# Optimization experiments

Measured on AMD Instinct MI355X. Metric: run time of the kernel, lower is better.

Reference implementation:

```python
import jax, jax.numpy as jnp
import numpy as np

IMG = 640
NUM_CLASSES = 80
STRIDES = (8, 16, 32)
CONF_THRESH = 0.05
NMS_THRESH = 0.5
C3, C4, C5 = 128, 256, 512
B = 4


def _conv(x, w, b, pad):
    # x: [B,Cin,H,W], w: [Cout,Cin,kh,kw]
    y = jax.lax.conv_general_dilated(x, w, (1, 1), [(pad, pad), (pad, pad)],
                                     dimension_numbers=('NCHW', 'OIHW', 'NCHW'))
    return y + b[None, :, None, None]


def _conv_act(x, w, b):
    return jax.nn.leaky_relu(_conv(x, w, b, 1), 0.1)


def _head(x, ws, bs):
    # ws: [4,256,256,3,3] stacked head convs (fixed count of 4)
    for i in range(ws.shape[0]):
        x = _conv_act(x, ws[i], bs[i])
    return x


def _up2(x):
    # nearest-neighbor upsample x2 (F.interpolate default)
    return jnp.repeat(jnp.repeat(x, 2, axis=2), 2, axis=3)


def _grid(stride):
    hs = IMG // stride
    gy, gx = jnp.meshgrid(jnp.arange(hs), jnp.arange(hs), indexing='ij')
    return jnp.stack([gx, gy], -1).reshape(-1, 2).astype(jnp.float32)  # [hs*ws,2]


def _fcos_dense(c3, c4, c5, params):
    (lat1_w, lat1_b, lat2_w, lat2_b, lat3_w, lat3_b,
     sm1_w, sm1_b, sm2_w, sm2_b, sm3_w, sm3_b,
     clsh_w, clsh_b, regh_w, regh_b,
     cls_det_w, cls_det_b, reg_det_w, reg_det_b, ctn_det_w, ctn_det_b) = params
    p5 = _conv(c5, lat3_w, lat3_b, 0)
    p5_up = _up2(p5)                      # upsample BEFORE smooth, as in source
    p5 = _conv(p5, sm3_w, sm3_b, 1)
    p4 = _conv(c4, lat2_w, lat2_b, 0) + p5_up
    p4_up = _up2(p4)
    p4 = _conv(p4, sm2_w, sm2_b, 1)
    p3 = _conv(_conv(c3, lat1_w, lat1_b, 0) + p4_up, sm1_w, sm1_b, 1)
    cls_all, box_all, ctn_all = [], [], []
    for p, s in zip((p3, p4, p5), STRIDES):
        bsz = p.shape[0]
        ch = _head(p, clsh_w, clsh_b)
        rh = _head(p, regh_w, regh_b)
        cls_i = jnp.transpose(_conv(ch, cls_det_w, cls_det_b, 0), (0, 2, 3, 1)).reshape(bsz, -1, NUM_CLASSES)
        reg_i = jnp.transpose(_conv(rh, reg_det_w, reg_det_b, 0), (0, 2, 3, 1)).reshape(bsz, -1, 4)
        ctn_i = jnp.transpose(_conv(rh, ctn_det_w, ctn_det_b, 0), (0, 2, 3, 1)).reshape(bsz, -1, 1)
        g = _grid(s)[None]                 # [1,HW,2]
        x1y1 = (g - jnp.exp(reg_i[..., :2])) * s
        x2y2 = (g + jnp.exp(reg_i[..., 2:])) * s
        cls_all.append(cls_i)
        box_all.append(jnp.concatenate([x1y1, x2y2], -1))
        ctn_all.append(ctn_i)
    return (jnp.concatenate(cls_all, 1), jnp.concatenate(box_all, 1), jnp.concatenate(ctn_all, 1))


def _nms_keep(boxes, scores, cls_inds):
    # Greedy per-class NMS, fixed-shape: returns keep mask in original order.
    N = boxes.shape[0]
    order = jnp.argsort(-scores)
    b = boxes[order]
    s = scores[order]
    c = cls_inds[order]
    x1, y1, x2, y2 = b[:, 0], b[:, 1], b[:, 2], b[:, 3]
    areas = (x2 - x1) * (y2 - y1)
    idx = jnp.arange(N)
    keep0 = s >= CONF_THRESH

    def body(i, keep):
        xx1 = jnp.maximum(x1[i], x1)
        yy1 = jnp.maximum(y1[i], y1)
        xx2 = jnp.minimum(x2[i], x2)
        yy2 = jnp.minimum(y2[i], y2)
        w = jnp.maximum(1e-28, xx2 - xx1)
        h = jnp.maximum(1e-28, yy2 - yy1)
        inter = w * h
        ovr = inter / (areas[i] + areas - inter)
        sup = keep[i] & (idx > i) & (c == c[i]) & (ovr > NMS_THRESH)
        return keep & ~sup

    keep = jax.lax.fori_loop(0, N, body, keep0)
    return jnp.zeros(N, bool).at[order].set(keep)


def setup_inputs() -> dict:
    key = jax.random.key(0)
    ks = iter(jax.random.split(key, 64))

    def wn(shape):
        fan_in = float(np.prod(shape[1:]))
        return jax.random.normal(next(ks), shape, jnp.float32) / np.sqrt(fan_in)

    def bz(n):
        return jnp.zeros((n,), jnp.float32)

    inp = {
        'c3': jax.random.normal(next(ks), (B, C3, 80, 80), jnp.float32),
        'c4': jax.random.normal(next(ks), (B, C4, 40, 40), jnp.float32),
        'c5': jax.random.normal(next(ks), (B, C5, 20, 20), jnp.float32),
        'lat1_w': wn((256, C3, 1, 1)), 'lat1_b': bz(256),
        'lat2_w': wn((256, C4, 1, 1)), 'lat2_b': bz(256),
        'lat3_w': wn((256, C5, 1, 1)), 'lat3_b': bz(256),
        'sm1_w': wn((256, 256, 3, 3)), 'sm1_b': bz(256),
        'sm2_w': wn((256, 256, 3, 3)), 'sm2_b': bz(256),
        'sm3_w': wn((256, 256, 3, 3)), 'sm3_b': bz(256),
        'clsh_w': jnp.stack([wn((256, 256, 3, 3)) for _ in range(4)]),
        'clsh_b': jnp.zeros((4, 256), jnp.float32),
        'regh_w': jnp.stack([wn((256, 256, 3, 3)) for _ in range(4)]),
        'regh_b': jnp.zeros((4, 256), jnp.float32),
        'cls_det_w': wn((NUM_CLASSES, 256, 1, 1)),
        'cls_det_b': jnp.full((NUM_CLASSES,), -np.log(99.0), jnp.float32),
        'reg_det_w': wn((4, 256, 1, 1)), 'reg_det_b': bz(4),
        'ctn_det_w': wn((1, 256, 1, 1)), 'ctn_det_b': bz(1),
    }
    return inp


def reference(c3, c4, c5, lat1_w, lat1_b, lat2_w, lat2_b, lat3_w, lat3_b,
              sm1_w, sm1_b, sm2_w, sm2_b, sm3_w, sm3_b,
              clsh_w, clsh_b, regh_w, regh_b,
              cls_det_w, cls_det_b, reg_det_w, reg_det_b, ctn_det_w, ctn_det_b):
    params = (lat1_w, lat1_b, lat2_w, lat2_b, lat3_w, lat3_b,
              sm1_w, sm1_b, sm2_w, sm2_b, sm3_w, sm3_b,
              clsh_w, clsh_b, regh_w, regh_b,
              cls_det_w, cls_det_b, reg_det_w, reg_det_b, ctn_det_w, ctn_det_b)
    cls_pred, box_pred, ctn_pred = _fcos_dense(c3, c4, c5, params)
    scores = jnp.sqrt(jax.nn.sigmoid(cls_pred) * jax.nn.sigmoid(ctn_pred))[0]  # [N,C]
    bboxes = jnp.clip(box_pred / IMG, 0.0, 1.0)[0]                              # [N,4]
    cls_inds = jnp.argmax(scores, axis=1)
    best = jnp.take_along_axis(scores, cls_inds[:, None], axis=1)[:, 0]
    keep = _nms_keep(bboxes, best, cls_inds)
    return bboxes, best, cls_inds.astype(jnp.int32), keep
```

## Files before the change

kernel.cpp:

```cpp
#include <hip/hip_runtime.h>
#include <stdint.h>

#define CONF_T 0.05f
#define NMS_T  0.5f
#define WMAX   132
#define WSTEP9 589824

typedef _Float16 f16x8 __attribute__((ext_vector_type(8)));
typedef _Float16 f16x2 __attribute__((ext_vector_type(2)));
typedef float    f32x4 __attribute__((ext_vector_type(4)));
#define MFMA16 __builtin_amdgcn_mfma_f32_16x16x32_f16

#define OFF_T3   0u
#define OFF_T4   1638400u
#define OFF_T5   2048000u
#define OFF_P3   2150400u
#define OFF_P4   3788800u
#define OFF_P5   4198400u
#define OFF_HA3  4300800u
#define OFF_HA4  5939200u
#define OFF_HA5  6348800u
#define OFF_HB3  6451200u
#define OFF_HB4  8089600u
#define OFF_HB5  8499200u
#define OFF_HD3  8601600u
#define OFF_HD4  10240000u
#define OFF_HD5  10649600u
#define OFF_CLS  10752000u
#define OFF_REG  11424000u
#define OFF_CTN  11457600u
#define OFF_W2H  11466000u
#define OFF_W2L  14710032u
#define WS_NEED  17954064u
#define POFF_KEYS  (OFF_T3 + 0u)
#define POFF_SCS   (OFF_T3 + 32768u)
#define POFF_CLSS  (OFF_T3 + 49152u)
#define POFF_IDXS  (OFF_T3 + 65536u)
#define POFF_GX1   (OFF_T3 + 81920u)
#define POFF_GY1   (OFF_T3 + 90320u)
#define POFF_GX2   (OFF_T3 + 98720u)
#define POFF_GY2   (OFF_T3 + 107120u)
#define POFF_GAR   (OFF_T3 + 115520u)
#define POFF_GIX   (OFF_T3 + 123920u)
#define POFF_NCNT  (OFF_T3 + 132320u)
#define POFF_NBASE (OFF_T3 + 132400u)
#define POFF_CROW  (OFF_T3 + 132480u)
#define POFF_NZ    (OFF_T3 + 140880u)
#define POFF_MASK  OFF_HA3

__launch_bounds__(256)
__global__ void conv1x1_kernel(const float* __restrict__ in, const float* __restrict__ w,
                               const float* __restrict__ b, float* __restrict__ out,
                               const float* __restrict__ add,
                               int Cin, int Cout, int NPX, int W, int outStride, int outBase)
{
    __shared__ float s_in[16][64];
    __shared__ float s_w[16][64];
    int t = threadIdx.x;
    int pxg = t & 31, cg = t >> 5;
    int px0 = blockIdx.x * 64;
    int co0 = blockIdx.y * 64;
    float acc[8][2];
#pragma unroll
    for (int c = 0; c < 8; ++c) { acc[c][0] = 0.f; acc[c][1] = 0.f; }
    int chunks = Cin >> 4;
    int wco = t >> 2, wpart = t & 3;
    for (int ch = 0; ch < chunks; ++ch) {
        int ci0 = ch << 4;
#pragma unroll
        for (int k = 0; k < 4; ++k) {
            int id = t + k * 256;
            int ci = id >> 6, pp = id & 63;
            int gp = px0 + pp;
            s_in[ci][pp] = (gp < NPX) ? in[(size_t)(ci0 + ci) * NPX + gp] : 0.f;
        }
        {
            int gco = co0 + wco;
            if (gco < Cout) {
                const float* run = w + (size_t)gco * Cin + ci0;
#pragma unroll
                for (int k = 0; k < 4; ++k) {
                    int e = wpart + 4 * k;
                    s_w[e][wco] = run[e];
                }
            } else {
#pragma unroll
                for (int k = 0; k < 4; ++k) s_w[wpart + 4 * k][wco] = 0.f;
            }
        }
        __syncthreads();
#pragma unroll
        for (int ci = 0; ci < 16; ++ci) {
            float i0 = s_in[ci][pxg * 2], i1 = s_in[ci][pxg * 2 + 1];
#pragma unroll
            for (int c = 0; c < 8; ++c) {
                float wv = s_w[ci][cg * 8 + c];
                acc[c][0] += wv * i0;
                acc[c][1] += wv * i1;
            }
        }
        __syncthreads();
    }
    for (int c = 0; c < 8; ++c) {
        int co = co0 + cg * 8 + c;
        if (co >= Cout) break;
        float bb = b[co];
#pragma unroll
        for (int j = 0; j < 2; ++j) {
            int p = px0 + pxg * 2 + j;
            if (p < NPX) {
                float v = acc[c][j] + bb;
                if (add) {
                    int y = p / W, x = p % W;
                    int Sp = W >> 1;
                    v += add[(size_t)co * (Sp * Sp) + (y >> 1) * Sp + (x >> 1)];
                }
                out[(size_t)co * outStride + outBase + p] = v;
            }
        }
    }
}

struct Det9 {
    const float* src[9]; const float* w[9]; const float* b[9];
    float*       dst[9];
    int cout[9], npx[9], obase[9], bstart[9], npxb[9];
};

__launch_bounds__(256)
__global__ void det1x1_fused(Det9 d)
{
    int bid = blockIdx.x;
    int q = 0;
#pragma unroll
    for (int i = 1; i < 9; ++i) if (bid >= d.bstart[i]) q = i;
    int local = bid - d.bstart[q];
    int coIdx = local / d.npxb[q];
    int pxIdx = local - coIdx * d.npxb[q];
    const float* in = d.src[q];
    const float* w  = d.w[q];
    const float* b  = d.b[q];
    float* out = d.dst[q];
    int Cout = d.cout[q], NPX = d.npx[q], outBase = d.obase[q];

    __shared__ float s_in[16][64];
    __shared__ float s_w[16][64];
    int t = threadIdx.x;
    int pxg = t & 31, cg = t >> 5;
    int px0 = pxIdx * 64;
    int co0 = coIdx * 64;
    float acc[8][2];
#pragma unroll
    for (int c = 0; c < 8; ++c) { acc[c][0] = 0.f; acc[c][1] = 0.f; }
    int wco = t >> 2, wpart = t & 3;
    for (int ch = 0; ch < 16; ++ch) {
        int ci0 = ch << 4;
#pragma unroll
        for (int k = 0; k < 4; ++k) {
            int id = t + k * 256;
            int ci = id >> 6, pp = id & 63;
            int gp = px0 + pp;
            s_in[ci][pp] = (gp < NPX) ? in[(size_t)(ci0 + ci) * NPX + gp] : 0.f;
        }
        {
            int gco = co0 + wco;
            if (gco < Cout) {
                const float* run = w + (size_t)gco * 256 + ci0;
#pragma unroll
                for (int k = 0; k < 4; ++k) {
                    int e = wpart + 4 * k;
                    s_w[e][wco] = run[e];
                }
            } else {
#pragma unroll
                for (int k = 0; k < 4; ++k) s_w[wpart + 4 * k][wco] = 0.f;
            }
        }
        __syncthreads();
#pragma unroll
        for (int ci = 0; ci < 16; ++ci) {
            float i0 = s_in[ci][pxg * 2], i1 = s_in[ci][pxg * 2 + 1];
#pragma unroll
            for (int c = 0; c < 8; ++c) {
                float wv = s_w[ci][cg * 8 + c];
                acc[c][0] += wv * i0;
                acc[c][1] += wv * i1;
            }
        }
        __syncthreads();
    }
    for (int c = 0; c < 8; ++c) {
        int co = co0 + cg * 8 + c;
        if (co >= Cout) break;
        float bb = b[co];
#pragma unroll
        for (int j = 0; j < 2; ++j) {
            int p = px0 + pxg * 2 + j;
            if (p < NPX) out[(size_t)co * 8400 + outBase + p] = acc[c][j] + bb;
        }
    }
}

__launch_bounds__(256)
__global__ void w2prep(const float* __restrict__ clsh_w, const float* __restrict__ regh_w,
                       const float* __restrict__ sm1_w, const float* __restrict__ sm2_w,
                       const float* __restrict__ sm3_w,
                       _Float16* __restrict__ WH, _Float16* __restrict__ WL)
{
    int idx = blockIdx.x * 256 + threadIdx.x;
    if (idx >= 11 * WSTEP9) return;
    int m = idx / WSTEP9, e = idx - m * WSTEP9;
    int tap = e / 65536;
    int r   = e - tap * 65536;
    int cob = r / 4096;
    int r2  = r - cob * 4096;
    int ck  = r2 / 512;
    int r3  = r2 - ck * 512;
    int lane = r3 / 8, el = r3 - (r3 / 8) * 8;
    int co = cob * 16 + (lane & 15);
    int ci = ck * 32 + (lane >> 4) * 8 + el;
    const float* srcb;
    if (m < 4)       srcb = clsh_w + (size_t)m * WSTEP9;
    else if (m < 8)  srcb = regh_w + (size_t)(m - 4) * WSTEP9;
    else if (m == 8) srcb = sm1_w;
    else if (m == 9) srcb = sm2_w;
    else             srcb = sm3_w;
    float f = srcb[(size_t)co * 2304 + ci * 9 + tap];
    _Float16 h = (_Float16)f;
    _Float16 l = (_Float16)(f - (float)h);
    WH[idx] = h; WL[idx] = l;
}

struct MC {
    const float*    src[2][3];
    float*          dst[2][3];
    const _Float16* wh[2][3];
    const _Float16* wl[2][3];
    const float*    bias[2][3];
    int act;
    int nbr;
};

__launch_bounds__(256)
__global__ void mconv3x3(MC p)
{
    __shared__ __align__(16) _Float16 SH[2][108 * 40];
    __shared__ __align__(16) _Float16 SL[2][108 * 40];
    int t = threadIdx.x;
    int NS = 4 * p.nbr;
    int bid = blockIdx.x;
    int slice = bid % NS;
    int sp = bid / NS;
    int br = slice % p.nbr;
    int co0 = (slice / p.nbr) * 64;
    int lvl = (sp < 100) ? 0 : (sp < 130) ? 1 : 2;
    int tloc = sp - ((lvl == 0) ? 0 : (lvl == 1) ? 100 : 130);
    int W = (lvl == 0) ? 80 : (lvl == 1) ? 40 : 20;
    int nTx = (lvl == 0) ? 5 : (lvl == 1) ? 3 : 2;
    int HW = W * W;
    int bx0 = (tloc % nTx) * 16, by0 = (tloc / nTx) * 4;
    const float* src = p.src[br][lvl];
    float* dst = p.dst[br][lvl];
    const _Float16* wh = p.wh[br][lvl];
    const _Float16* wl = p.wl[br][lvl];
    const float* bias = p.bias[br][lvl];

    int lane = t & 63, wid = t >> 6;
    int cw = wid & 1, pw = wid >> 1;
    int colc = lane & 15, g = lane >> 4;

    int sgo[7], sla[7];
#pragma unroll
    for (int k = 0; k < 7; ++k) {
        int s2 = t + k * 256;
        sgo[k] = -1; sla[k] = 0;
        if (s2 < 1728) {
            int ci2 = s2 / 108, cell = s2 - ci2 * 108;
            int r = cell / 18, c = cell - r * 18;
            sla[k] = cell * 40 + ci2 * 2;
            int gy = by0 - 1 + r, gx = bx0 - 1 + c;
            if (gy >= 0 && gy < W && gx >= 0 && gx < W)
                sgo[k] = (ci2 * 2) * HW + gy * W + gx;
        }
    }

    f32x4 acc[2][2];
#pragma unroll
    for (int mi = 0; mi < 2; ++mi)
#pragma unroll
        for (int ny = 0; ny < 2; ++ny) acc[mi][ny] = (f32x4)0.f;

#pragma unroll
    for (int k = 0; k < 7; ++k) {
        if (t + k * 256 < 1728) {
            float v0 = 0.f, v1 = 0.f;
            if (sgo[k] >= 0) { v0 = src[sgo[k]]; v1 = src[sgo[k] + HW]; }
            _Float16 h0 = (_Float16)v0, h1 = (_Float16)v1;
            _Float16 l0 = (_Float16)(v0 - (float)h0), l1 = (_Float16)(v1 - (float)h1);
            f16x2 ph = {h0, h1}, pl = {l0, l1};
            *(f16x2*)&SH[0][sla[k]] = ph;
            *(f16x2*)&SL[0][sla[k]] = pl;
        }
    }
    __syncthreads();

    int cob0 = (co0 + cw * 32) >> 4;
    auto aoff = [&](int ckk, int tap, int mi) -> size_t {
        return ((size_t)((tap * 16 + cob0 + mi) * 8 + ckk)) * 512 + lane * 8;
    };
    f16x8 Ah0[3], Al0[3], Ah1[3], Al1[3];
    {
        size_t a0 = aoff(0, 0, 0), a1 = aoff(0, 0, 1);
        Ah0[0] = *(const f16x8*)(wh + a0); Al0[0] = *(const f16x8*)(wl + a0);
        Ah1[0] = *(const f16x8*)(wh + a1); Al1[0] = *(const f16x8*)(wl + a1);
        a0 = aoff(0, 1, 0); a1 = aoff(0, 1, 1);
        Ah0[1] = *(const f16x8*)(wh + a0); Al0[1] = *(const f16x8*)(wl + a0);
        Ah1[1] = *(const f16x8*)(wh + a1); Al1[1] = *(const f16x8*)(wl + a1);
    }
    for (int ck = 0; ck < 8; ++ck) {
        const _Float16* sh  = SH[ck & 1];
        const _Float16* sl_ = SL[ck & 1];
        float pv[14];
        bool pf = (ck < 7);
        if (pf) {
            const float* sb = src + (size_t)(ck + 1) * 32 * HW;
#pragma unroll
            for (int k = 0; k < 7; ++k) {
                pv[2 * k] = 0.f; pv[2 * k + 1] = 0.f;
                if (t + k * 256 < 1728 && sgo[k] >= 0) {
                    pv[2 * k] = sb[sgo[k]]; pv[2 * k + 1] = sb[sgo[k] + HW];
                }
            }
        }
#pragma unroll
        for (int tap = 0; tap < 9; ++tap) {
            int ky = tap / 3, kx = tap - ky * 3;
            int slot = tap % 3;
            int nsl  = (tap + 2) % 3;
            int pck = ck, ptap = tap + 2;
            if (ptap >= 9) { ptap -= 9; if (pf) pck = ck + 1; }
            size_t an0 = aoff(pck, ptap, 0), an1 = aoff(pck, ptap, 1);
            Ah0[nsl] = *(const f16x8*)(wh + an0);
            Al0[nsl] = *(const f16x8*)(wl + an0);
            Ah1[nsl] = *(const f16x8*)(wh + an1);
            Al1[nsl] = *(const f16x8*)(wl + an1);
#pragma unroll
            for (int ny = 0; ny < 2; ++ny) {
                int cell = (pw * 2 + ny + ky) * 18 + colc + kx;
                f16x8 bh = *(const f16x8*)(sh  + cell * 40 + g * 8);
                f16x8 bl = *(const f16x8*)(sl_ + cell * 40 + g * 8);
                acc[0][ny] = MFMA16(Ah0[slot], bh, acc[0][ny], 0, 0, 0);
                acc[1][ny] = MFMA16(Ah1[slot], bh, acc[1][ny], 0, 0, 0);
                acc[0][ny] = MFMA16(Ah0[slot], bl, acc[0][ny], 0, 0, 0);
                acc[1][ny] = MFMA16(Ah1[slot], bl, acc[1][ny], 0, 0, 0);
                acc[0][ny] = MFMA16(Al0[slot], bh, acc[0][ny], 0, 0, 0);
                acc[1][ny] = MFMA16(Al1[slot], bh, acc[1][ny], 0, 0, 0);
            }
        }
        if (pf) {
            _Float16* nh = SH[(ck + 1) & 1];
            _Float16* nl = SL[(ck + 1) & 1];
#pragma unroll
            for (int k = 0; k < 7; ++k) {
                if (t + k * 256 < 1728) {
                    float v0 = pv[2 * k], v1 = pv[2 * k + 1];
                    _Float16 h0 = (_Float16)v0, h1 = (_Float16)v1;
                    _Float16 l0 = (_Float16)(v0 - (float)h0), l1 = (_Float16)(v1 - (float)h1);
                    f16x2 ph = {h0, h1}, pl = {l0, l1};
                    *(f16x2*)&nh[sla[k]] = ph;
                    *(f16x2*)&nl[sla[k]] = pl;
                }
            }
        }
        __syncthreads();
    }

    int x = bx0 + colc;
    if (x < W) {
#pragma unroll
        for (int mi = 0; mi < 2; ++mi) {
            int cob = co0 + cw * 32 + mi * 16 + g * 4;
#pragma unroll
            for (int ny = 0; ny < 2; ++ny) {
                int y = by0 + pw * 2 + ny;
#pragma unroll
                for (int i = 0; i < 4; ++i) {
                    int co = cob + i;
                    float v = acc[mi][ny][i] + bias[co];
                    if (p.act) v = (v >= 0.f) ? v : 0.1f * v;
                    dst[(size_t)co * HW + y * W + x] = v;
                }
            }
        }
    }
}

__launch_bounds__(256)
__global__ void decode_kernel(const float* __restrict__ cls, const float* __restrict__ reg,
                              const float* __restrict__ ctn, float* __restrict__ out,
                              unsigned long long* __restrict__ keys)
{
    int p = blockIdx.x * 256 + threadIdx.x;
    if (p >= 16384) return;
    if (p >= 8400) { keys[p] = ~0ull; return; }
    int base, hs; float s;
    if (p < 6400)      { base = 0;    hs = 80; s = 8.f;  }
    else if (p < 8000) { base = 6400; hs = 40; s = 16.f; }
    else               { base = 8000; hs = 20; s = 32.f; }
    int local = p - base;
    float gx = (float)(local % hs), gy = (float)(local / hs);
    float ct = ctn[p];
    float sct = 1.f / (1.f + expf(-ct));
    float best = -1.f; int arg = 0;
    for (int c = 0; c < 80; ++c) {
        float v = cls[(size_t)c * 8400 + p];
        float sv = 1.f / (1.f + expf(-v));
        float sc = sqrtf(sv * sct);
        if (sc > best) { best = sc; arg = c; }
    }
    float r0 = reg[0 * 8400 + p], r1 = reg[1 * 8400 + p];
    float r2 = reg[2 * 8400 + p], r3 = reg[3 * 8400 + p];
    float x1 = (gx - expf(r0)) * s / 640.f;
    float y1 = (gy - expf(r1)) * s / 640.f;
    float x2 = (gx + expf(r2)) * s / 640.f;
    float y2 = (gy + expf(r3)) * s / 640.f;
    x1 = fminf(fmaxf(x1, 0.f), 1.f);
    y1 = fminf(fmaxf(y1, 0.f), 1.f);
    x2 = fminf(fmaxf(x2, 0.f), 1.f);
    y2 = fminf(fmaxf(y2, 0.f), 1.f);
    out[p * 4 + 0] = x1; out[p * 4 + 1] = y1;
    out[p * 4 + 2] = x2; out[p * 4 + 3] = y2;
    out[33600 + p] = best;
    out[42000 + p] = (float)arg;
    out[50400 + p] = 0.f;
    unsigned int ub = __float_as_uint(best);
    keys[p] = ((unsigned long long)(~ub) << 32) | (unsigned int)p;
}

__launch_bounds__(256)
__global__ void bitonic_local(unsigned long long* __restrict__ keys, unsigned kmerge)
{
    __shared__ unsigned long long sk[2048];
    int t = threadIdx.x;
    unsigned base = blockIdx.x * 2048u;
#pragma unroll
    for (int m = 0; m < 8; ++m) sk[t + m * 256] = keys[base + t + m * 256];
    __syncthreads();
    if (kmerge == 0u) {
        for (unsigned k = 2; k <= 2048u; k <<= 1) {
            for (unsigned j = k >> 1; j > 0; j >>= 1) {
#pragma unroll
                for (int pp = 0; pp < 4; ++pp) {
                    unsigned p = (unsigned)t + pp * 256u;
                    unsigned li = ((p & ~(j - 1)) << 1) | (p & (j - 1));
                    unsigned gi = base + li;
                    bool up = ((gi & k) == 0);
                    unsigned long long a = sk[li], b = sk[li + j];
                    if ((a > b) == up) { sk[li] = b; sk[li + j] = a; }
                }
                __syncthreads();
            }
        }
    } else {
        unsigned k = kmerge;
        for (unsigned j = 1024; j > 0; j >>= 1) {
#pragma unroll
            for (int pp = 0; pp < 4; ++pp) {
                unsigned p = (unsigned)t + pp * 256u;
                unsigned li = ((p & ~(j - 1)) << 1) | (p & (j - 1));
                unsigned gi = base + li;
                bool up = ((gi & k) == 0);
                unsigned long long a = sk[li], b = sk[li + j];
                if ((a > b) == up) { sk[li] = b; sk[li + j] = a; }
            }
            __syncthreads();
        }
    }
#pragma unroll
    for (int m = 0; m < 8; ++m) keys[base + t + m * 256] = sk[t + m * 256];
}

__launch_bounds__(256)
__global__ void bitonic_global(unsigned long long* __restrict__ keys, unsigned k, unsigned j)
{
    unsigned p = blockIdx.x * 256u + threadIdx.x;
    unsigned i = ((p & ~(j - 1)) << 1) | (p & (j - 1));
    bool up = ((i & k) == 0);
    unsigned long long a = keys[i], b = keys[i + j];
    if ((a > b) == up) { keys[i] = b; keys[i + j] = a; }
}

__launch_bounds__(256)
__global__ void sorted_aux(const unsigned long long* __restrict__ keys,
                           const float* __restrict__ out,
                           float* __restrict__ scs, int* __restrict__ clss,
                           int* __restrict__ idxs)
{
    int i = blockIdx.x * 256 + threadIdx.x;
    if (i >= 16384) return;
    unsigned long long key = keys[i];
    unsigned ub = ~(unsigned)(key >> 32);
    float sc = __uint_as_float(ub);
    unsigned idx = (unsigned)(key & 0xffffffffu);
    int cl = -1;
    if (idx < 8400u) cl = (int)out[42000 + idx];
    else sc = 0.f;
    scs[i] = sc; clss[i] = cl; idxs[i] = (int)idx;
}

__launch_bounds__(256)
__global__ void compact_cls(const float* __restrict__ scs, const int* __restrict__ clss,
                            const int* __restrict__ idxs, const float* __restrict__ outbuf,
                            float* __restrict__ GX1, float* __restrict__ GY1,
                            float* __restrict__ GX2, float* __restrict__ GY2,
                            float* __restrict__ GAR, int* __restrict__ GIX,
                            int* __restrict__ CROW,
                            int* __restrict__ NCOUNT, int* __restrict__ NBASE)
{
    int c = blockIdx.x, t = threadIdx.x;
    __shared__ int s_red[2];
    __shared__ int s_wtot[4];
    int cb = 0, co = 0;
    for (int i = t; i < 16384; i += 256) {
        float sc = scs[i]; int cl = clss[i];
        if (sc >= CONF_T && cl >= 0) { cb += (cl < c); co += (cl == c); }
    }
    if (t == 0) { s_red[0] = 0; s_red[1] = 0; }
    __syncthreads();
    atomicAdd(&s_red[0], cb);
    atomicAdd(&s_red[1], co);
    __syncthreads();
    int base = s_red[0], n = s_red[1];
    if (t == 0) { NCOUNT[c] = n; NBASE[c] = base; }

    int rank = 0;
    for (int st = 0; st < 16384; st += 256) {
        int i = st + t;
        float sc = scs[i]; int cl = clss[i];
        bool flag = (sc >= CONF_T && cl == c);
        unsigned long long m = __ballot(flag);
        int lane = t & 63, wv = t >> 6;
        if (lane == 0) s_wtot[wv] = __popcll(m);
        __syncthreads();
        int off = rank;
        for (int w = 0; w < wv; ++w) off += s_wtot[w];
        int tot = s_wtot[0] + s_wtot[1] + s_wtot[2] + s_wtot[3];
        if (flag) {
            int pos = off + __popcll(m & ((1ull << lane) - 1ull));
            int idx = idxs[i];
            float x1 = outbuf[idx * 4 + 0], y1 = outbuf[idx * 4 + 1];
            float x2 = outbuf[idx * 4 + 2], y2 = outbuf[idx * 4 + 3];
            GX1[base + pos] = x1; GY1[base + pos] = y1;
            GX2[base + pos] = x2; GY2[base + pos] = y2;
            GAR[base + pos] = (x2 - x1) * (y2 - y1);
            GIX[base + pos] = idx;
            CROW[base + pos] = c;
        }
        rank += tot;
        __syncthreads();
    }
}

__launch_bounds__(256)
__global__ void nms_mask(const float* __restrict__ GX1, const float* __restrict__ GY1,
                         const float* __restrict__ GX2, const float* __restrict__ GY2,
                         const float* __restrict__ GAR,
                         const int* __restrict__ CROW,
                         const int* __restrict__ NCOUNT, const int* __restrict__ NBASE,
                         unsigned long long* __restrict__ MASK,
                         unsigned long long* __restrict__ NZ)
{
    int lane = threadIdx.x & 63, wid = threadIdx.x >> 6;
    int gr = blockIdx.x * 4 + wid;
    int tot = NBASE[79] + NCOUNT[79];
    if (gr >= tot) return;
    int c = CROW[gr];
    int base = NBASE[c], n = NCOUNT[c];
    int r = gr - base;
    float rx1 = GX1[gr], ry1 = GY1[gr];
    float rx2 = GX2[gr], ry2 = GY2[gr];
    float rar = GAR[gr];
    int Wc = (n + 63) >> 6;
    unsigned long long nz0 = 0ull, nz1 = 0ull, nz2 = 0ull;
    for (int w = 0; w < Wc; ++w) {
        int jb = w * 64;
        unsigned long long m = 0ull;
        if (jb + 63 > r) {
            int j = jb + lane;
            bool pred = false;
            if (j > r && j < n) {
                float xx1 = fmaxf(rx1, GX1[base + j]);
                float yy1 = fmaxf(ry1, GY1[base + j]);
                float xx2 = fminf(rx2, GX2[base + j]);
                float yy2 = fminf(ry2, GY2[base + j]);
                float ww = fmaxf(1e-28f, xx2 - xx1);
                float hh = fmaxf(1e-28f, yy2 - yy1);
                float inter = ww * hh;
                float ovr = inter / (rar + GAR[base + j] - inter);
                pred = (ovr > NMS_T);
            }
            m = __ballot(pred);
        }
        if (lane == 0) {
            MASK[(size_t)gr * WMAX + w] = m;
            if (m) {
                if (w < 64)       nz0 |= 1ull << w;
                else if (w < 128) nz1 |= 1ull << (w - 64);
                else              nz2 |= 1ull << (w - 128);
            }
        }
    }
    if (lane == 0) {
        NZ[(size_t)gr * 4 + 0] = nz0;
        NZ[(size_t)gr * 4 + 1] = nz1;
        NZ[(size_t)gr * 4 + 2] = nz2;
    }
}

__launch_bounds__(256)
__global__ void nms_scan(const unsigned long long* __restrict__ MASK,
                         const unsigned long long* __restrict__ NZ,
                         const int* __restrict__ GIX,
                         const int* __restrict__ NCOUNT, const int* __restrict__ NBASE,
                         float* __restrict__ keep)
{
    int c = blockIdx.x, t = threadIdx.x;
    int n = NCOUNT[c];
    if (n == 0) return;
    int base = NBASE[c];
    int Wc = (n + 63) >> 6;
    __shared__ unsigned long long remv[WMAX];
    __shared__ unsigned long long sdiag[64];
    __shared__ unsigned long long s_am;
    __shared__ int s_rows[64];
    __shared__ int s_na;
    for (int w = t; w < Wc; w += 256) remv[w] = 0ull;
    __syncthreads();
    for (int i0 = 0; i0 < n; i0 += 64) {
        int rows = min(64, n - i0);
        int wq = i0 >> 6;
        if (t < rows) sdiag[t] = MASK[(size_t)(base + i0 + t) * WMAX + wq];
        __syncthreads();
        if (t == 0) {
            unsigned long long live = (rows < 64) ? ((1ull << rows) - 1ull) : ~0ull;
            live &= ~remv[wq];
            unsigned long long am = 0ull;
            int na = 0;
            while (live) {
                int rr = __ffsll((unsigned long long)live) - 1;
                am |= 1ull << rr;
                s_rows[na++] = rr;
                live &= ~sdiag[rr];
                live &= ~(1ull << rr);
            }
            s_am = am; s_na = na;
        }
        __syncthreads();
        unsigned long long am = s_am;
        int na = s_na;
        if (t < na) {
            int gr = base + i0 + s_rows[t];
#pragma unroll
            for (int part = 0; part < 3; ++part) {
                unsigned long long nz = NZ[(size_t)gr * 4 + part];
                while (nz) {
                    int b = __ffsll((unsigned long long)nz) - 1;
                    nz &= nz - 1ull;
                    int w = part * 64 + b;
                    atomicOr(&remv[w], MASK[(size_t)gr * WMAX + w]);
                }
            }
        }
        __syncthreads();
        if (t < rows && ((am >> t) & 1ull)) keep[GIX[base + i0 + t]] = 1.0f;
        __syncthreads();
    }
}

extern "C" void kernel_launch(void* const* d_in, const int* in_sizes, int n_in,
                              void* d_out, int out_size, void* d_ws, size_t ws_size,
                              hipStream_t stream)
{
    const float* c3      = (const float*)d_in[0];
    const float* c4      = (const float*)d_in[1];
    const float* c5      = (const float*)d_in[2];
    const float* lat1_w  = (const float*)d_in[3];
    const float* lat1_b  = (const float*)d_in[4];
    const float* lat2_w  = (const float*)d_in[5];
    const float* lat2_b  = (const float*)d_in[6];
    const float* lat3_w  = (const float*)d_in[7];
    const float* lat3_b  = (const float*)d_in[8];
    const float* sm1_w   = (const float*)d_in[9];
    const float* sm1_b   = (const float*)d_in[10];
    const float* sm2_w   = (const float*)d_in[11];
    const float* sm2_b   = (const float*)d_in[12];
    const float* sm3_w   = (const float*)d_in[13];
    const float* sm3_b   = (const float*)d_in[14];
    const float* clsh_w  = (const float*)d_in[15];
    const float* clsh_b  = (const float*)d_in[16];
    const float* regh_w  = (const float*)d_in[17];
    const float* regh_b  = (const float*)d_in[18];
    const float* clsd_w  = (const float*)d_in[19];
    const float* clsd_b  = (const float*)d_in[20];
    const float* regd_w  = (const float*)d_in[21];
    const float* regd_b  = (const float*)d_in[22];
    const float* ctnd_w  = (const float*)d_in[23];
    const float* ctnd_b  = (const float*)d_in[24];

    float* ws = (float*)d_ws;
    float* T3 = ws + OFF_T3;  float* T4 = ws + OFF_T4;  float* T5 = ws + OFF_T5;
    float* P3 = ws + OFF_P3;  float* P4 = ws + OFF_P4;  float* P5 = ws + OFF_P5;
    float* HA3 = ws + OFF_HA3; float* HA4 = ws + OFF_HA4; float* HA5 = ws + OFF_HA5;
    float* HB3 = ws + OFF_HB3; float* HB4 = ws + OFF_HB4; float* HB5 = ws + OFF_HB5;
    float* HD3 = ws + OFF_HD3; float* HD4 = ws + OFF_HD4; float* HD5 = ws + OFF_HD5;
    float* CLS = ws + OFF_CLS; float* REG = ws + OFF_REG; float* CTN = ws + OFF_CTN;
    _Float16* WH = (_Float16*)(ws + OFF_W2H);
    _Float16* WL = (_Float16*)(ws + OFF_W2L);
    unsigned long long* KEYS = (unsigned long long*)(ws + POFF_KEYS);
    float* SCS = ws + POFF_SCS;
    int* CLSS = (int*)(ws + POFF_CLSS);
    int* IDXS = (int*)(ws + POFF_IDXS);
    float* GX1 = ws + POFF_GX1; float* GY1 = ws + POFF_GY1;
    float* GX2 = ws + POFF_GX2; float* GY2 = ws + POFF_GY2;
    float* GAR = ws + POFF_GAR;
    int* GIX = (int*)(ws + POFF_GIX);
    int* CROW = (int*)(ws + POFF_CROW);
    int* NCOUNT = (int*)(ws + POFF_NCNT);
    int* NBASE  = (int*)(ws + POFF_NBASE);
    unsigned long long* NZ = (unsigned long long*)(ws + POFF_NZ);
    unsigned long long* MASK = (unsigned long long*)(ws + POFF_MASK);

    float* out = (float*)d_out;
    dim3 blk(256);

    w2prep<<<dim3((11 * WSTEP9 + 255) / 256), blk, 0, stream>>>(
        clsh_w, regh_w, sm1_w, sm2_w, sm3_w, WH, WL);

    conv1x1_kernel<<<dim3(7, 4), blk, 0, stream>>>(c5, lat3_w, lat3_b, T5, nullptr,
                                                   512, 256, 400, 20, 400, 0);
    conv1x1_kernel<<<dim3(25, 4), blk, 0, stream>>>(c4, lat2_w, lat2_b, T4, T5,
                                                    256, 256, 1600, 40, 1600, 0);
    conv1x1_kernel<<<dim3(100, 4), blk, 0, stream>>>(c3, lat1_w, lat1_b, T3, T4,
                                                     128, 256, 6400, 80, 6400, 0);
    {
        MC mc{};
        float* sT[3] = {T3, T4, T5};
        float* sP[3] = {P3, P4, P5};
        const float* sB[3] = {sm1_b, sm2_b, sm3_b};
        for (int l = 0; l < 3; ++l) {
            mc.src[0][l] = sT[l]; mc.dst[0][l] = sP[l];
            mc.wh[0][l] = WH + (size_t)(8 + l) * WSTEP9;
            mc.wl[0][l] = WL + (size_t)(8 + l) * WSTEP9;
            mc.bias[0][l] = sB[l];
        }
        mc.act = 0; mc.nbr = 1;
        mconv3x3<<<dim3(140 * 4), blk, 0, stream>>>(mc);
    }
    {
        float* clsS[3][5] = { {P3, HA3, HB3, HA3, HB3},
                              {P4, HA4, HB4, HA4, HB4},
                              {P5, HA5, HB5, HA5, HB5} };
        float* regS[3][5] = { {P3, T3,  HD3, T3,  HD3},
                              {P4, T4,  HD4, T4,  HD4},
                              {P5, T5,  HD5, T5,  HD5} };
        for (int i = 0; i < 4; ++i) {
            MC mc{};
            for (int l = 0; l < 3; ++l) {
                mc.src[0][l] = clsS[l][i]; mc.dst[0][l] = clsS[l][i + 1];
                mc.src[1][l] = regS[l][i]; mc.dst[1][l] = regS[l][i + 1];
                mc.wh[0][l] = WH + (size_t)i * WSTEP9;
                mc.wl[0][l] = WL + (size_t)i * WSTEP9;
                mc.wh[1][l] = WH + (size_t)(4 + i) * WSTEP9;
                mc.wl[1][l] = WL + (size_t)(4 + i) * WSTEP9;
                mc.bias[0][l] = clsh_b + i * 256;
                mc.bias[1][l] = regh_b + i * 256;
            }
            mc.act = 1; mc.nbr = 2;
            mconv3x3<<<dim3(140 * 8), blk, 0, stream>>>(mc);
        }
    }

    {
        Det9 d;
        const float* feats[3][2] = { {HB3, HD3}, {HB4, HD4}, {HB5, HD5} };
        int   npx[3]   = {6400, 1600, 400};
        int   obase[3] = {0, 6400, 8000};
        int q = 0, bacc = 0;
        for (int l = 0; l < 3; ++l) {
            d.src[q] = feats[l][0]; d.w[q] = clsd_w; d.b[q] = clsd_b; d.dst[q] = CLS;
            d.cout[q] = 80; d.npx[q] = npx[l]; d.obase[q] = obase[l];
            d.bstart[q] = bacc; d.npxb[q] = (npx[l] + 63) / 64;
            bacc += d.npxb[q] * 2; ++q;
            d.src[q] = feats[l][1]; d.w[q] = regd_w; d.b[q] = regd_b; d.dst[q] = REG;
            d.cout[q] = 4; d.npx[q] = npx[l]; d.obase[q] = obase[l];
            d.bstart[q] = bacc; d.npxb[q] = (npx[l] + 63) / 64;
            bacc += d.npxb[q]; ++q;
            d.src[q] = feats[l][1]; d.w[q] = ctnd_w; d.b[q] = ctnd_b; d.dst[q] = CTN;
            d.cout[q] = 1; d.npx[q] = npx[l]; d.obase[q] = obase[l];
            d.bstart[q] = bacc; d.npxb[q] = (npx[l] + 63) / 64;
            bacc += d.npxb[q]; ++q;
        }
        det1x1_fused<<<dim3(bacc), blk, 0, stream>>>(d);
    }

    decode_kernel<<<dim3(64), blk, 0, stream>>>(CLS, REG, CTN, out, KEYS);

    bitonic_local<<<dim3(8), blk, 0, stream>>>(KEYS, 0u);
    bitonic_global<<<dim3(32), blk, 0, stream>>>(KEYS, 4096u, 2048u);
    bitonic_local<<<dim3(8), blk, 0, stream>>>(KEYS, 4096u);
    bitonic_global<<<dim3(32), blk, 0, stream>>>(KEYS, 8192u, 4096u);
    bitonic_global<<<dim3(32), blk, 0, stream>>>(KEYS, 8192u, 2048u);
    bitonic_local<<<dim3(8), blk, 0, stream>>>(KEYS, 8192u);
    bitonic_global<<<dim3(32), blk, 0, stream>>>(KEYS, 16384u, 8192u);
    bitonic_global<<<dim3(32), blk, 0, stream>>>(KEYS, 16384u, 4096u);
    bitonic_global<<<dim3(32), blk, 0, stream>>>(KEYS, 16384u, 2048u);
    bitonic_local<<<dim3(8), blk, 0, stream>>>(KEYS, 16384u);

    sorted_aux<<<dim3(64), blk, 0, stream>>>(KEYS, out, SCS, CLSS, IDXS);
    compact_cls<<<dim3(80), blk, 0, stream>>>(SCS, CLSS, IDXS, out,
                                              GX1, GY1, GX2, GY2, GAR, GIX, CROW,
                                              NCOUNT, NBASE);
    nms_mask<<<dim3(2100), blk, 0, stream>>>(GX1, GY1, GX2, GY2, GAR, CROW,
                                             NCOUNT, NBASE, MASK, NZ);
    nms_scan<<<dim3(80), blk, 0, stream>>>(MASK, NZ, GIX, NCOUNT, NBASE, out + 50400);
}
```

Measured before the change: 935.6 us.

## Store intermediate conv activations as pre-split fp16 hi/lo channel pairs

The 3x3 conv kernel can now write its output as packed fp16 high and low halves for channel pairs instead of fp32 planes. The next conv then loads these words straight into shared memory without converting again. This removes the repeated fp32-to-split-fp16 conversion during staging and keeps global traffic the same size (two 32-bit words per channel pair). The smooth convs and the first three head layers emit the pair layout, and the last head layer still writes fp32 for the detector kernel. The change relies on every buffer being large enough for the hi and lo planes placed at the 128*HW offset.

```diff
diff --git a/kernel.cpp b/kernel.cpp
--- a/kernel.cpp
+++ b/kernel.cpp
@@ -239,6 +239,8 @@
     const float*    bias[2][3];
     int act;
     int nbr;
+    int inPairs;
+    int outPairs;
 };
 
 __launch_bounds__(256)
@@ -264,23 +266,28 @@
     const _Float16* wh = p.wh[br][lvl];
     const _Float16* wl = p.wl[br][lvl];
     const float* bias = p.bias[br][lvl];
+    const unsigned* PHsrc = (const unsigned*)src;
+    const unsigned* PLsrc = PHsrc + (size_t)128 * HW;
 
     int lane = t & 63, wid = t >> 6;
     int cw = wid & 1, pw = wid >> 1;
     int colc = lane & 15, g = lane >> 4;
 
-    int sgo[7], sla[7];
+    int sgo[7], sci[7], sla[7];
 #pragma unroll
     for (int k = 0; k < 7; ++k) {
         int s2 = t + k * 256;
-        sgo[k] = -1; sla[k] = 0;
+        sgo[k] = -1; sci[k] = 0; sla[k] = 0;
         if (s2 < 1728) {
             int ci2 = s2 / 108, cell = s2 - ci2 * 108;
             int r = cell / 18, c = cell - r * 18;
             sla[k] = cell * 40 + ci2 * 2;
+            sci[k] = ci2;
             int gy = by0 - 1 + r, gx = bx0 - 1 + c;
             if (gy >= 0 && gy < W && gx >= 0 && gx < W)
-                sgo[k] = (ci2 * 2) * HW + gy * W + gx;
+                sgo[k] = gy * W + gx;
+        } else {
+            sla[k] = -1;
         }
     }
 
@@ -292,14 +299,23 @@
 
 #pragma unroll
     for (int k = 0; k < 7; ++k) {
-        if (t + k * 256 < 1728) {
-            float v0 = 0.f, v1 = 0.f;
-            if (sgo[k] >= 0) { v0 = src[sgo[k]]; v1 = src[sgo[k] + HW]; }
-            _Float16 h0 = (_Float16)v0, h1 = (_Float16)v1;
-            _Float16 l0 = (_Float16)(v0 - (float)h0), l1 = (_Float16)(v1 - (float)h1);
-            f16x2 ph = {h0, h1}, pl = {l0, l1};
-            *(f16x2*)&SH[0][sla[k]] = ph;
-            *(f16x2*)&SL[0][sla[k]] = pl;
+        if (sla[k] >= 0) {
+            unsigned hw_ = 0u, lw_ = 0u;
+            if (sgo[k] >= 0) {
+                if (p.inPairs) {
+                    hw_ = PHsrc[(size_t)sci[k] * HW + sgo[k]];
+                    lw_ = PLsrc[(size_t)sci[k] * HW + sgo[k]];
+                } else {
+                    float v0 = src[(size_t)(sci[k] * 2) * HW + sgo[k]];
+                    float v1 = src[(size_t)(sci[k] * 2 + 1) * HW + sgo[k]];
+                    _Float16 h0 = (_Float16)v0, h1 = (_Float16)v1;
+                    _Float16 l0 = (_Float16)(v0 - (float)h0), l1 = (_Float16)(v1 - (float)h1);
+                    f16x2 ph = {h0, h1}, pl = {l0, l1};
+                    hw_ = *(unsigned*)&ph; lw_ = *(unsigned*)&pl;
+                }
+            }
+            *(unsigned*)&SH[0][sla[k]] = hw_;
+            *(unsigned*)&SL[0][sla[k]] = lw_;
         }
     }
     __syncthreads();
@@ -320,21 +336,34 @@
     for (int ck = 0; ck < 8; ++ck) {
         const _Float16* sh  = SH[ck & 1];
         const _Float16* sl_ = SL[ck & 1];
-        float pv[14];
+        unsigned pv[14];
         bool pf = (ck < 7);
         if (pf) {
-            const float* sb = src + (size_t)(ck + 1) * 32 * HW;
-#pragma unroll
-            for (int k = 0; k < 7; ++k) {
-                pv[2 * k] = 0.f; pv[2 * k + 1] = 0.f;
-                if (t + k * 256 < 1728 && sgo[k] >= 0) {
-                    pv[2 * k] = sb[sgo[k]]; pv[2 * k + 1] = sb[sgo[k] + HW];
+            if (p.inPairs) {
+                const unsigned* ph = PHsrc + (size_t)(ck + 1) * 16 * HW;
+                const unsigned* pl = PLsrc + (size_t)(ck + 1) * 16 * HW;
+#pragma unroll
+                for (int k = 0; k < 7; ++k) {
+                    pv[2 * k] = 0u; pv[2 * k + 1] = 0u;
+                    if (sla[k] >= 0 && sgo[k] >= 0) {
+                        pv[2 * k]     = ph[(size_t)sci[k] * HW + sgo[k]];
+                        pv[2 * k + 1] = pl[(size_t)sci[k] * HW + sgo[k]];
+                    }
+                }
+            } else {
+                const float* sb = src + (size_t)(ck + 1) * 32 * HW;
+#pragma unroll
+                for (int k = 0; k < 7; ++k) {
+                    pv[2 * k] = 0u; pv[2 * k + 1] = 0u;
+                    if (sla[k] >= 0 && sgo[k] >= 0) {
+                        pv[2 * k]     = __float_as_uint(sb[(size_t)(sci[k] * 2) * HW + sgo[k]]);
+                        pv[2 * k + 1] = __float_as_uint(sb[(size_t)(sci[k] * 2 + 1) * HW + sgo[k]]);
+                    }
                 }
             }
         }
 #pragma unroll
         for (int tap = 0; tap < 9; ++tap) {
-            int ky = tap / 3, kx = tap - ky * 3;
             int slot = tap % 3;
             int nsl  = (tap + 2) % 3;
             int pck = ck, ptap = tap + 2;
@@ -344,6 +373,7 @@
             Al0[nsl] = *(const f16x8*)(wl + an0);
             Ah1[nsl] = *(const f16x8*)(wh + an1);
             Al1[nsl] = *(const f16x8*)(wl + an1);
+            int ky = tap / 3, kx = tap - ky * 3;
 #pragma unroll
             for (int ny = 0; ny < 2; ++ny) {
                 int cell = (pw * 2 + ny + ky) * 18 + colc + kx;
@@ -360,15 +390,26 @@
         if (pf) {
             _Float16* nh = SH[(ck + 1) & 1];
             _Float16* nl = SL[(ck + 1) & 1];
-#pragma unroll
-            for (int k = 0; k < 7; ++k) {
-                if (t + k * 256 < 1728) {
-                    float v0 = pv[2 * k], v1 = pv[2 * k + 1];
-                    _Float16 h0 = (_Float16)v0, h1 = (_Float16)v1;
-                    _Float16 l0 = (_Float16)(v0 - (float)h0), l1 = (_Float16)(v1 - (float)h1);
-                    f16x2 ph = {h0, h1}, pl = {l0, l1};
-                    *(f16x2*)&nh[sla[k]] = ph;
-                    *(f16x2*)&nl[sla[k]] = pl;
+            if (p.inPairs) {
+#pragma unroll
+                for (int k = 0; k < 7; ++k) {
+                    if (sla[k] >= 0) {
+                        *(unsigned*)&nh[sla[k]] = pv[2 * k];
+                        *(unsigned*)&nl[sla[k]] = pv[2 * k + 1];
+                    }
+                }
+            } else {
+#pragma unroll
+                for (int k = 0; k < 7; ++k) {
+                    if (sla[k] >= 0) {
+                        float v0 = __uint_as_float(pv[2 * k]);
+                        float v1 = __uint_as_float(pv[2 * k + 1]);
+                        _Float16 h0 = (_Float16)v0, h1 = (_Float16)v1;
+                        _Float16 l0 = (_Float16)(v0 - (float)h0), l1 = (_Float16)(v1 - (float)h1);
+                        f16x2 ph = {h0, h1}, pl = {l0, l1};
+                        *(unsigned*)&nh[sla[k]] = *(unsigned*)&ph;
+                        *(unsigned*)&nl[sla[k]] = *(unsigned*)&pl;
+                    }
                 }
             }
         }
@@ -377,18 +418,37 @@
 
     int x = bx0 + colc;
     if (x < W) {
+        unsigned* PHdst = (unsigned*)dst;
+        unsigned* PLdst = PHdst + (size_t)128 * HW;
 #pragma unroll
         for (int mi = 0; mi < 2; ++mi) {
             int cob = co0 + cw * 32 + mi * 16 + g * 4;
 #pragma unroll
             for (int ny = 0; ny < 2; ++ny) {
                 int y = by0 + pw * 2 + ny;
+                int off = y * W + x;
+                float v[4];
 #pragma unroll
                 for (int i = 0; i < 4; ++i) {
-                    int co = cob + i;
-                    float v = acc[mi][ny][i] + bias[co];
-                    if (p.act) v = (v >= 0.f) ? v : 0.1f * v;
-                    dst[(size_t)co * HW + y * W + x] = v;
+                    float vv = acc[mi][ny][i] + bias[cob + i];
+                    if (p.act) vv = (vv >= 0.f) ? vv : 0.1f * vv;
+                    v[i] = vv;
+                }
+                if (p.outPairs) {
+#pragma unroll
+                    for (int pr = 0; pr < 2; ++pr) {
+                        float v0 = v[2 * pr], v1 = v[2 * pr + 1];
+                        _Float16 h0 = (_Float16)v0, h1 = (_Float16)v1;
+                        _Float16 l0 = (_Float16)(v0 - (float)h0), l1 = (_Float16)(v1 - (float)h1);
+                        f16x2 ph = {h0, h1}, pl = {l0, l1};
+                        size_t pidx = (size_t)(cob / 2 + pr) * HW + off;
+                        PHdst[pidx] = *(unsigned*)&ph;
+                        PLdst[pidx] = *(unsigned*)&pl;
+                    }
+                } else {
+#pragma unroll
+                    for (int i = 0; i < 4; ++i)
+                        dst[(size_t)(cob + i) * HW + off] = v[i];
                 }
             }
         }
@@ -753,7 +813,7 @@
             mc.wl[0][l] = WL + (size_t)(8 + l) * WSTEP9;
             mc.bias[0][l] = sB[l];
         }
-        mc.act = 0; mc.nbr = 1;
+        mc.act = 0; mc.nbr = 1; mc.inPairs = 0; mc.outPairs = 1;
         mconv3x3<<<dim3(140 * 4), blk, 0, stream>>>(mc);
     }
     {
@@ -776,6 +836,8 @@
                 mc.bias[1][l] = regh_b + i * 256;
             }
             mc.act = 1; mc.nbr = 2;
+            mc.inPairs = 1;
+            mc.outPairs = (i < 3) ? 1 : 0;
             mconv3x3<<<dim3(140 * 8), blk, 0, stream>>>(mc);
         }
     }
```

Result: slower. 993.2 us (+6.2%).

## Halve 3x3 conv spatial tile to two rows, one 16-channel block per wave

Applied to the files above, without the earlier changes.

The 3x3 MFMA conv tile shrinks from 16x4 to 16x2 output pixels per block, and each wave now owns a distinct 16-output-channel block instead of a 32-channel by 2-row share. The block count doubles and LDS per block drops, which should raise occupancy and spread work over more CUs. In exchange, each wave fetches its own weights with less reuse across pixels, and halo overhead per output pixel goes up (4 input rows for 2 output rows).

```diff
diff --git a/kernel.cpp b/kernel.cpp
--- a/kernel.cpp
+++ b/kernel.cpp
@@ -244,8 +244,8 @@
 __launch_bounds__(256)
 __global__ void mconv3x3(MC p)
 {
-    __shared__ __align__(16) _Float16 SH[2][108 * 40];
-    __shared__ __align__(16) _Float16 SL[2][108 * 40];
+    __shared__ __align__(16) _Float16 SH[2][72 * 40];
+    __shared__ __align__(16) _Float16 SL[2][72 * 40];
     int t = threadIdx.x;
     int NS = 4 * p.nbr;
     int bid = blockIdx.x;
@@ -253,12 +253,12 @@
     int sp = bid / NS;
     int br = slice % p.nbr;
     int co0 = (slice / p.nbr) * 64;
-    int lvl = (sp < 100) ? 0 : (sp < 130) ? 1 : 2;
-    int tloc = sp - ((lvl == 0) ? 0 : (lvl == 1) ? 100 : 130);
+    int lvl = (sp < 200) ? 0 : (sp < 260) ? 1 : 2;
+    int tloc = sp - ((lvl == 0) ? 0 : (lvl == 1) ? 200 : 260);
     int W = (lvl == 0) ? 80 : (lvl == 1) ? 40 : 20;
     int nTx = (lvl == 0) ? 5 : (lvl == 1) ? 3 : 2;
     int HW = W * W;
-    int bx0 = (tloc % nTx) * 16, by0 = (tloc / nTx) * 4;
+    int bx0 = (tloc % nTx) * 16, by0 = (tloc / nTx) * 2;
     const float* src = p.src[br][lvl];
     float* dst = p.dst[br][lvl];
     const _Float16* wh = p.wh[br][lvl];
@@ -266,16 +266,15 @@
     const float* bias = p.bias[br][lvl];
 
     int lane = t & 63, wid = t >> 6;
-    int cw = wid & 1, pw = wid >> 1;
     int colc = lane & 15, g = lane >> 4;
 
-    int sgo[7], sla[7];
-#pragma unroll
-    for (int k = 0; k < 7; ++k) {
+    int sgo[5], sla[5];
+#pragma unroll
+    for (int k = 0; k < 5; ++k) {
         int s2 = t + k * 256;
         sgo[k] = -1; sla[k] = 0;
-        if (s2 < 1728) {
-            int ci2 = s2 / 108, cell = s2 - ci2 * 108;
+        if (s2 < 1152) {
+            int ci2 = s2 / 72, cell = s2 - ci2 * 72;
             int r = cell / 18, c = cell - r * 18;
             sla[k] = cell * 40 + ci2 * 2;
             int gy = by0 - 1 + r, gx = bx0 - 1 + c;
@@ -284,15 +283,12 @@
         }
     }
 
-    f32x4 acc[2][2];
-#pragma unroll
-    for (int mi = 0; mi < 2; ++mi)
-#pragma unroll
-        for (int ny = 0; ny < 2; ++ny) acc[mi][ny] = (f32x4)0.f;
-
-#pragma unroll
-    for (int k = 0; k < 7; ++k) {
-        if (t + k * 256 < 1728) {
+    f32x4 acc[2];
+    acc[0] = (f32x4)0.f; acc[1] = (f32x4)0.f;
+
+#pragma unroll
+    for (int k = 0; k < 5; ++k) {
+        if (t + k * 256 < 1152) {
             float v0 = 0.f, v1 = 0.f;
             if (sgo[k] >= 0) { v0 = src[sgo[k]]; v1 = src[sgo[k] + HW]; }
             _Float16 h0 = (_Float16)v0, h1 = (_Float16)v1;
@@ -304,30 +300,28 @@
     }
     __syncthreads();
 
-    int cob0 = (co0 + cw * 32) >> 4;
-    auto aoff = [&](int ckk, int tap, int mi) -> size_t {
-        return ((size_t)((tap * 16 + cob0 + mi) * 8 + ckk)) * 512 + lane * 8;
+    int cob0 = (co0 >> 4) + wid;
+    auto aoff = [&](int ckk, int tap) -> size_t {
+        return ((size_t)((tap * 16 + cob0) * 8 + ckk)) * 512 + lane * 8;
     };
-    f16x8 Ah0[3], Al0[3], Ah1[3], Al1[3];
+    f16x8 Ah[3], Al[3];
     {
-        size_t a0 = aoff(0, 0, 0), a1 = aoff(0, 0, 1);
-        Ah0[0] = *(const f16x8*)(wh + a0); Al0[0] = *(const f16x8*)(wl + a0);
-        Ah1[0] = *(const f16x8*)(wh + a1); Al1[0] = *(const f16x8*)(wl + a1);
-        a0 = aoff(0, 1, 0); a1 = aoff(0, 1, 1);
-        Ah0[1] = *(const f16x8*)(wh + a0); Al0[1] = *(const f16x8*)(wl + a0);
-        Ah1[1] = *(const f16x8*)(wh + a1); Al1[1] = *(const f16x8*)(wl + a1);
+        size_t a0 = aoff(0, 0);
+        Ah[0] = *(const f16x8*)(wh + a0); Al[0] = *(const f16x8*)(wl + a0);
+        a0 = aoff(0, 1);
+        Ah[1] = *(const f16x8*)(wh + a0); Al[1] = *(const f16x8*)(wl + a0);
     }
     for (int ck = 0; ck < 8; ++ck) {
         const _Float16* sh  = SH[ck & 1];
         const _Float16* sl_ = SL[ck & 1];
-        float pv[14];
+        float pv[10];
         bool pf = (ck < 7);
         if (pf) {
             const float* sb = src + (size_t)(ck + 1) * 32 * HW;
 #pragma unroll
-            for (int k = 0; k < 7; ++k) {
+            for (int k = 0; k < 5; ++k) {
                 pv[2 * k] = 0.f; pv[2 * k + 1] = 0.f;
-                if (t + k * 256 < 1728 && sgo[k] >= 0) {
+                if (t + k * 256 < 1152 && sgo[k] >= 0) {
                     pv[2 * k] = sb[sgo[k]]; pv[2 * k + 1] = sb[sgo[k] + HW];
                 }
             }
@@ -339,30 +333,25 @@
             int nsl  = (tap + 2) % 3;
             int pck = ck, ptap = tap + 2;
             if (ptap >= 9) { ptap -= 9; if (pf) pck = ck + 1; }
-            size_t an0 = aoff(pck, ptap, 0), an1 = aoff(pck, ptap, 1);
-            Ah0[nsl] = *(const f16x8*)(wh + an0);
-            Al0[nsl] = *(const f16x8*)(wl + an0);
-            Ah1[nsl] = *(const f16x8*)(wh + an1);
-            Al1[nsl] = *(const f16x8*)(wl + an1);
+            size_t an = aoff(pck, ptap);
+            Ah[nsl] = *(const f16x8*)(wh + an);
+            Al[nsl] = *(const f16x8*)(wl + an);
 #pragma unroll
             for (int ny = 0; ny < 2; ++ny) {
-                int cell = (pw * 2 + ny + ky) * 18 + colc + kx;
+                int cell = (ny + ky) * 18 + colc + kx;
                 f16x8 bh = *(const f16x8*)(sh  + cell * 40 + g * 8);
                 f16x8 bl = *(const f16x8*)(sl_ + cell * 40 + g * 8);
-                acc[0][ny] = MFMA16(Ah0[slot], bh, acc[0][ny], 0, 0, 0);
-                acc[1][ny] = MFMA16(Ah1[slot], bh, acc[1][ny], 0, 0, 0);
-                acc[0][ny] = MFMA16(Ah0[slot], bl, acc[0][ny], 0, 0, 0);
-                acc[1][ny] = MFMA16(Ah1[slot], bl, acc[1][ny], 0, 0, 0);
-                acc[0][ny] = MFMA16(Al0[slot], bh, acc[0][ny], 0, 0, 0);
-                acc[1][ny] = MFMA16(Al1[slot], bh, acc[1][ny], 0, 0, 0);
+                acc[ny] = MFMA16(Ah[slot], bh, acc[ny], 0, 0, 0);
+                acc[ny] = MFMA16(Ah[slot], bl, acc[ny], 0, 0, 0);
+                acc[ny] = MFMA16(Al[slot], bh, acc[ny], 0, 0, 0);
             }
         }
         if (pf) {
             _Float16* nh = SH[(ck + 1) & 1];
             _Float16* nl = SL[(ck + 1) & 1];
 #pragma unroll
-            for (int k = 0; k < 7; ++k) {
-                if (t + k * 256 < 1728) {
+            for (int k = 0; k < 5; ++k) {
+                if (t + k * 256 < 1152) {
                     float v0 = pv[2 * k], v1 = pv[2 * k + 1];
                     _Float16 h0 = (_Float16)v0, h1 = (_Float16)v1;
                     _Float16 l0 = (_Float16)(v0 - (float)h0), l1 = (_Float16)(v1 - (float)h1);
@@ -377,19 +366,16 @@
 
     int x = bx0 + colc;
     if (x < W) {
-#pragma unroll
-        for (int mi = 0; mi < 2; ++mi) {
-            int cob = co0 + cw * 32 + mi * 16 + g * 4;
-#pragma unroll
-            for (int ny = 0; ny < 2; ++ny) {
-                int y = by0 + pw * 2 + ny;
-#pragma unroll
-                for (int i = 0; i < 4; ++i) {
-                    int co = cob + i;
-                    float v = acc[mi][ny][i] + bias[co];
-                    if (p.act) v = (v >= 0.f) ? v : 0.1f * v;
-                    dst[(size_t)co * HW + y * W + x] = v;
-                }
+        int cob = co0 + wid * 16 + g * 4;
+#pragma unroll
+        for (int ny = 0; ny < 2; ++ny) {
+            int y = by0 + ny;
+#pragma unroll
+            for (int i = 0; i < 4; ++i) {
+                int co = cob + i;
+                float v = acc[ny][i] + bias[co];
+                if (p.act) v = (v >= 0.f) ? v : 0.1f * v;
+                dst[(size_t)co * HW + y * W + x] = v;
             }
         }
     }
@@ -754,7 +740,7 @@
             mc.bias[0][l] = sB[l];
         }
         mc.act = 0; mc.nbr = 1;
-        mconv3x3<<<dim3(140 * 4), blk, 0, stream>>>(mc);
+        mconv3x3<<<dim3(280 * 4), blk, 0, stream>>>(mc);
     }
     {
         float* clsS[3][5] = { {P3, HA3, HB3, HA3, HB3},
@@ -776,7 +762,7 @@
                 mc.bias[1][l] = regh_b + i * 256;
             }
             mc.act = 1; mc.nbr = 2;
-            mconv3x3<<<dim3(140 * 8), blk, 0, stream>>>(mc);
+            mconv3x3<<<dim3(280 * 8), blk, 0, stream>>>(mc);
         }
     }
 
```

New measurement: 851.3 us (median of 2 runs). 9.0% less time.
